# Performance work log

Hardware: AMD Instinct MI355X
Metric: run time of the kernel (lower is better)

## Reference

```python
import jax, jax.numpy as jnp
import numpy as np

N_NODES = 50000
N_EDGES = 1600000
NFEAT = 512
NHID = 64
H1 = 8      # nheads[0]
H2 = 1      # nheads[1]
NCLASS = 16
ALPHA = 0.2  # leaky_relu negative slope


def setup_inputs() -> dict:
    key = jax.random.key(0)
    ks = jax.random.split(key, 6)
    x = jax.random.normal(ks[0], (N_NODES, NFEAT), jnp.float32)
    edge_index = jax.random.randint(ks[1], (2, N_EDGES), 0, N_NODES, jnp.int32)

    def glorot(k, shape):
        fan_in, fan_out = shape[-2], shape[-1]
        std = (2.0 / (fan_in + fan_out)) ** 0.5
        return jax.random.normal(k, shape, jnp.float32) * std

    W1 = glorot(ks[2], (H1, NFEAT, NHID))
    a1 = jax.random.normal(ks[3], (H1, 2 * NHID), jnp.float32) * 0.1
    W2 = glorot(ks[4], (H2, NHID * H1, NCLASS))
    a2 = jax.random.normal(ks[5], (H2, 2 * NCLASS), jnp.float32) * 0.1
    return {"x": x, "edge_index": edge_index, "W1": W1, "a1": a1, "W2": W2, "a2": a2}


def _spgat_head(x, W, a, src, dst, n_nodes, apply_elu):
    # Sparse GAT head (pyGAT SpGraphAttentionLayer, eval mode / no dropout).
    h = x @ W                              # [N, F']
    f = W.shape[1]
    # a . [h_src || h_dst] decomposed into per-node scores (same math, no [E,2F'] concat)
    s_src = h @ a[:f]                      # [N]
    s_dst = h @ a[f:]                      # [N]
    logits = s_src[src] + s_dst[dst]       # [E]
    e = jnp.exp(-jax.nn.leaky_relu(logits, ALPHA))  # edge_e = exp(-leakyrelu(...)) > 0
    rowsum = jax.ops.segment_sum(e, src, num_segments=n_nodes)            # [N]
    agg = jax.ops.segment_sum(e[:, None] * h[dst], src, num_segments=n_nodes)  # [N, F']
    h_prime = agg / rowsum[:, None]
    return jax.nn.elu(h_prime) if apply_elu else h_prime


def reference(x, edge_index, W1, a1, W2, a2):
    src, dst = edge_index[0], edge_index[1]
    n = x.shape[0]
    # Layer 1: H1 heads, concat=True (elu inside each head), concatenated on features
    h = jnp.concatenate(
        [_spgat_head(x, W1[i], a1[i], src, dst, n, True) for i in range(W1.shape[0])],
        axis=1,
    )  # [N, H1*NHID]
    # Layer 2: H2 heads, concat=False, stacked then averaged
    outs = jnp.stack(
        [_spgat_head(h, W2[i], a2[i], src, dst, n, False) for i in range(W2.shape[0])],
        axis=2,
    )  # [N, NCLASS, H2]
    out = jnp.mean(outs, axis=2)
    return jax.nn.log_softmax(jax.nn.elu(out), axis=1)
```

## Files before the change

### kernel.cpp

```cpp
#include <hip/hip_runtime.h>

#define NN 50000
#define NE 1600000
#define NFEAT 512
#define NHID 64
#define H1 8
#define NCLASS 16
#define ALPHA 0.2f

#define BUCKETS 391
#define CAP 6144
#define EPB 4096
#define PASSA_BLKS 391
#define PASSB_BLKS 391
#define PACK_BLKS 1024
#define PACK2_BLKS 32
#define X8_BLKS 6250
#define GEMMB 391
#define NROW_PAD 50048

typedef __attribute__((ext_vector_type(8))) short short8;
typedef __attribute__((ext_vector_type(4))) float floatx4;
typedef __attribute__((ext_vector_type(2))) float floatx2;
typedef __attribute__((ext_vector_type(2))) long longx2;

__device__ __forceinline__ float elu_f(float x) { return x > 0.0f ? x : __expf(x) - 1.0f; }
__device__ __forceinline__ float edge_w(float logit) {
    return __expf(-fmaxf(logit, ALPHA * logit));
}
__device__ __forceinline__ ushort f2bf(float f) {
    uint u = __float_as_uint(f);
    return (ushort)((u + 0x7FFFu + ((u >> 16) & 1)) >> 16);
}
__device__ __forceinline__ uint packbf2(float lo, float hi) {
    return (uint)f2bf(lo) | ((uint)f2bf(hi) << 16);
}
__device__ __forceinline__ float bf2f(ushort v) { return __uint_as_float((uint)v << 16); }
__device__ __forceinline__ unsigned char f2fp8(float v) {
    return (unsigned char)(__builtin_amdgcn_cvt_pk_fp8_f32(v, v, 0, false) & 0xFF);
}
__device__ __forceinline__ uint pack4fp8(float a, float b, float c, float d) {
    uint u = __builtin_amdgcn_cvt_pk_fp8_f32(a, b, 0, false);
    return __builtin_amdgcn_cvt_pk_fp8_f32(c, d, u, true);
}

#define GLD16(g, l)                                                              \
    __builtin_amdgcn_global_load_lds(                                            \
        (const __attribute__((address_space(1))) unsigned int*)(g),              \
        (__attribute__((address_space(3))) unsigned int*)(l), 16, 0, 0)

__device__ __forceinline__ int scan256x(int v, int tid, int* wsum, int* tot) {
    int s = v;
#pragma unroll
    for (int o = 1; o < 64; o <<= 1) {
        int u = __shfl_up(s, o);
        if ((tid & 63) >= o) s += u;
    }
    __syncthreads();
    if ((tid & 63) == 63) wsum[tid >> 6] = s;
    __syncthreads();
    int off = 0, t = 0;
#pragma unroll
    for (int i = 0; i < 4; i++) {
        int x = wsum[i];
        if (i < (tid >> 6)) off += x;
        t += x;
    }
    *tot = t;
    return s - v + off;
}

__device__ __forceinline__ int scan512x(int v, int tid, int* wsum, int* tot) {
    int s = v;
#pragma unroll
    for (int o = 1; o < 64; o <<= 1) {
        int u = __shfl_up(s, o);
        if ((tid & 63) >= o) s += u;
    }
    __syncthreads();
    if ((tid & 63) == 63) wsum[tid >> 6] = s;
    __syncthreads();
    int off = 0, t = 0;
#pragma unroll
    for (int i = 0; i < 8; i++) {
        int x = wsum[i];
        if (i < (tid >> 6)) off += x;
        t += x;
    }
    *tot = t;
    return s - v + off;
}

__global__ __launch_bounds__(256) void prep_k(const float* __restrict__ W1,
                                              unsigned char* __restrict__ Wt8,
                                              const float* __restrict__ W2,
                                              ushort* __restrict__ W2tb,
                                              const float* __restrict__ x,
                                              unsigned char* x8,
                                              const int* __restrict__ ei,
                                              int* __restrict__ bucket_cnt,
                                              uint* __restrict__ staging) {
    int b = blockIdx.x;
    if (b < PACK_BLKS) {
        int i = b * 256 + threadIdx.x;
        int c = i >> 9, o = i & 511;
        int c6 = o >> 6, qhi = (o >> 4) & 3, kb = (o >> 3) & 1, bb = o & 7;
        int quad = qhi ^ ((c >> 1) & 3);
        int k = c6 * 64 + kb * 32 + quad * 8 + bb;
        Wt8[i] = f2fp8(W1[((c >> 6) * 512 + k) * 64 + (c & 63)]);
        return;
    }
    if (b < PACK_BLKS + PACK2_BLKS) {
        int i = (b - PACK_BLKS) * 256 + threadIdx.x;
        int c = i >> 9, f = i & 511;
        W2tb[i] = f2bf(W2[f * 16 + c]);
        return;
    }
    if (b < PACK_BLKS + PACK2_BLKS + X8_BLKS) {
        int i = (b - PACK_BLKS - PACK2_BLKS) * 256 + threadIdx.x;
        int row = i >> 5;
        int o0 = (i & 31) * 16;
        int c6 = o0 >> 6;
        int qhi = (o0 >> 4) & 3;
        int quad = qhi ^ ((row >> 1) & 3);
        const float* xp = x + (size_t)row * 512 + c6 * 64 + quad * 8;
        float4 v0 = *(const float4*)xp;
        float4 v1 = *(const float4*)(xp + 4);
        float4 v2 = *(const float4*)(xp + 32);
        float4 v3 = *(const float4*)(xp + 36);
        uint4 ov;
        ov.x = pack4fp8(v0.x, v0.y, v0.z, v0.w);
        ov.y = pack4fp8(v1.x, v1.y, v1.z, v1.w);
        ov.z = pack4fp8(v2.x, v2.y, v2.z, v2.w);
        ov.w = pack4fp8(v3.x, v3.y, v3.z, v3.w);
        *(uint4*)(x8 + (size_t)row * 512 + o0) = ov;
        return;
    }
    __shared__ int histA[BUCKETS];
    __shared__ int exclA[BUCKETS];
    __shared__ int baseA[BUCKETS];
    __shared__ int wsumA[4];
    __shared__ uint ebuf[EPB];
    const int blk = b - PACK_BLKS - PACK2_BLKS - X8_BLKS;
    const int t = threadIdx.x;
    const int e0 = blk * EPB;
    const int cntb = min(EPB, NE - e0);
    for (int i = t; i < BUCKETS; i += 256) histA[i] = 0;
    __syncthreads();
    int br[16]; uint pay[16];
#pragma unroll
    for (int i = 0; i < 16; i++) {
        int e = e0 + i * 256 + t;
        br[i] = -1;
        if (e < NE) {
            int s = ei[e], d = ei[NE + e];
            int bu = s >> 7;
            pay[i] = ((uint)bu << 23) | ((uint)(s & 127) << 16) | (uint)d;
            br[i] = (bu << 12) | atomicAdd(&histA[bu], 1);
        }
    }
    __syncthreads();
    int tot0, tot1;
    int v0 = histA[t];
    int v1 = (t + 256 < BUCKETS) ? histA[t + 256] : 0;
    int p0 = scan256x(v0, t, wsumA, &tot0);
    int p1 = scan256x(v1, t, wsumA, &tot1);
    exclA[t] = p0;
    if (t + 256 < BUCKETS) exclA[t + 256] = p1 + tot0;
    __syncthreads();
    for (int i = t; i < BUCKETS; i += 256) {
        int c = histA[i];
        if (c > 0) baseA[i] = atomicAdd(&bucket_cnt[i], c);
    }
#pragma unroll
    for (int i = 0; i < 16; i++)
        if (br[i] >= 0) ebuf[exclA[br[i] >> 12] + (br[i] & 4095)] = pay[i];
    __syncthreads();
    for (int j = t; j < cntb; j += 256) {
        uint v = ebuf[j];
        int bu = v >> 23;
        int pos = baseA[bu] + (j - exclA[bu]);
        staging[(size_t)bu * CAP + pos] = v;
    }
}

__global__ __launch_bounds__(512) void passb_gemm1_k(const int* __restrict__ bucket_cnt,
                                                     const uint* __restrict__ staging,
                                                     ushort* __restrict__ csru,
                                                     int* __restrict__ rowptr,
                                                     const unsigned char* __restrict__ Wt8,
                                                     const float* __restrict__ a1,
                                                     unsigned char* h8x8,
                                                     float* __restrict__ s1s,
                                                     float* __restrict__ s1d) {
    __shared__ unsigned char shmem[40960];
    const int tid = threadIdx.x;

    if (blockIdx.x < PASSB_BLKS) {
        int* hist2 = (int*)shmem;
        int* excl2 = hist2 + 128;
        int* cur2 = excl2 + 128;
        int* wsum2 = cur2 + 128;
        __shared__ int sbs;
        const int b = blockIdx.x;
        const int cnt = bucket_cnt[b];
        const uint* sg = staging + (size_t)b * CAP;
        if (tid < 128) { hist2[tid] = 0; cur2[tid] = 0; }
        if (tid < 64) {
            int c[7]; int s0 = 0;
#pragma unroll
            for (int i = 0; i < 7; i++) {
                int bi = tid * 7 + i;
                c[i] = (bi < BUCKETS) ? bucket_cnt[bi] : 0;
                s0 += c[i];
            }
            int sc = s0;
#pragma unroll
            for (int o = 1; o < 64; o <<= 1) {
                int u = __shfl_up(sc, o);
                if (tid >= o) sc += u;
            }
            int run = sc - s0;
            if (tid == b / 7) {
                int part = run;
                for (int i = 0; i < b % 7; i++) part += c[i];
                sbs = part;
            }
        }
        if (b == 0 && tid == 0) rowptr[NN] = NE;
        __syncthreads();
        const int sbase = sbs;
        for (int e = tid; e < cnt; e += 512) atomicAdd(&hist2[(sg[e] >> 16) & 127], 1);
        __syncthreads();
        int v = (tid < 128) ? hist2[tid] : 0;
        int tot;
        int ex = scan512x(v, tid, wsum2, &tot);
        if (tid < 128) {
            excl2[tid] = ex;
            int n = b * 128 + tid;
            if (n < NN) rowptr[n] = sbase + ex;
        }
        __syncthreads();
        for (int e = tid; e < cnt; e += 512) {
            uint u = sg[e];
            int sl = (u >> 16) & 127;
            int pos = excl2[sl] + atomicAdd(&cur2[sl], 1);
            csru[sbase + pos] = (ushort)(u & 0xFFFF);
        }
        return;
    }

    unsigned char* As = shmem;
    unsigned char* Bs = shmem + 8192;
    const int gb = blockIdx.x - PASSB_BLKS;
    const int row0 = gb * 128;
    const int wv = tid >> 6, lane = tid & 63;
    const int l16 = lane & 15, quad = lane >> 4;
    const int qoff = ((quad ^ ((l16 >> 1) & 3)) << 4);
    const int mA = wv * 16 + (lane >> 2);
    const int offA = (lane & 3) * 16;
    const unsigned char* gA = h8x8 + (size_t)(row0 + mA) * 512 + offA;
    const unsigned char* gB0 = Wt8 + (size_t)(0 * 128 + mA) * 512 + offA;
    const unsigned char* gB1 = Wt8 + (size_t)(1 * 128 + mA) * 512 + offA;
    const unsigned char* gB2 = Wt8 + (size_t)(2 * 128 + mA) * 512 + offA;
    const unsigned char* gB3 = Wt8 + (size_t)(3 * 128 + mA) * 512 + offA;

    floatx4 acc[32];
#pragma unroll
    for (int ct = 0; ct < 32; ct++) acc[ct] = (floatx4){0.f, 0.f, 0.f, 0.f};

    for (int k0 = 0; k0 < 512; k0 += 64) {
        GLD16(gA + k0, As + wv * 1024);
        GLD16(gB0 + k0, Bs + wv * 1024);
        GLD16(gB1 + k0, Bs + 8192 + wv * 1024);
        GLD16(gB2 + k0, Bs + 16384 + wv * 1024);
        GLD16(gB3 + k0, Bs + 24576 + wv * 1024);
        __syncthreads();
        longx2 av = *(const longx2*)(As + (wv * 16 + l16) * 64 + qoff);
        const unsigned char* bp = Bs + l16 * 64 + qoff;
#pragma unroll
        for (int ct = 0; ct < 32; ct++) {
            longx2 bv = *(const longx2*)(bp + ct * 1024);
            acc[ct] = __builtin_amdgcn_mfma_f32_16x16x32_fp8_fp8(av.x, bv.x, acc[ct], 0, 0, 0);
            acc[ct] = __builtin_amdgcn_mfma_f32_16x16x32_fp8_fp8(av.y, bv.y, acc[ct], 0, 0, 0);
        }
        __syncthreads();
    }

    const int rbase = row0 + wv * 16 + quad * 4;
#pragma unroll
    for (int hh = 0; hh < 8; hh++) {
        float ss[4] = {0.f, 0.f, 0.f, 0.f}, sd[4] = {0.f, 0.f, 0.f, 0.f};
#pragma unroll
        for (int c4 = 0; c4 < 4; c4++) {
            int ct = hh * 4 + c4;
            int colg = ct * 16 + l16;
            float avs = a1[hh * 128 + c4 * 16 + l16];
            float avd = a1[hh * 128 + 64 + c4 * 16 + l16];
#pragma unroll
            for (int r = 0; r < 4; r++) {
                float v = acc[ct][r];
                ss[r] += v * avs;
                sd[r] += v * avd;
                int row = rbase + r;
                if (row < NN) h8x8[(size_t)row * 512 + colg] = f2fp8(v);
            }
        }
#pragma unroll
        for (int r = 0; r < 4; r++) {
            float a_ = ss[r], b_ = sd[r];
#pragma unroll
            for (int o = 1; o < 16; o <<= 1) {
                a_ += __shfl_xor(a_, o);
                b_ += __shfl_xor(b_, o);
            }
            int row = rbase + r;
            if (l16 == 0 && row < NN) {
                s1s[row * 8 + hh] = a_;
                s1d[row * 8 + hh] = b_;
            }
        }
    }
}

__global__ __launch_bounds__(256) void agg1f_k(const int* __restrict__ rowptr,
                                               const ushort* __restrict__ csru,
                                               const float* __restrict__ s1s,
                                               const float* __restrict__ s1d,
                                               const uint2* __restrict__ hb8,
                                               const ushort* __restrict__ W2tb,
                                               const float* __restrict__ a2,
                                               ushort* __restrict__ h2b,
                                               float* __restrict__ s2s,
                                               float* __restrict__ s2d) {
    __shared__ ushort Ash[16 * 512];
    unsigned char* ashb = (unsigned char*)Ash;
    const int tid = threadIdx.x;
    const int wv = tid >> 6, lane = tid & 63;
    const int n0 = blockIdx.x * 4;
    const int n = n0 + wv;
    const int head8 = lane >> 3;
    const int hb = head8 << 3;
    const int esub = lane & 7;
    const int beg = rowptr[n];
    const int deg = rowptr[n + 1] - beg;
    const float ssrc = s1s[n * 8 + head8];
    floatx2 acc[4] = {};
    float rsum = 0.f;

    const int G = (deg + 7) >> 3;
    const int dm1 = deg - 1;
    if (G > 0) {
        int dA = csru[beg + min(esub, dm1)];
        float tw = s1d[dA * 8 + head8];
        for (int g = 0; g < G; g++) {
            uint2 v[8];
#pragma unroll
            for (int j = 0; j < 8; j++) {
                int dj = __shfl(dA, j);
                v[j] = hb8[(uint)dj * 64 + lane];
            }
            int dAn = csru[beg + min(g * 8 + 8 + esub, dm1)];
            float twn = s1d[dAn * 8 + head8];
            float w = (g * 8 + esub <= dm1) ? edge_w(ssrc + tw) : 0.f;
            rsum += w;
#pragma unroll
            for (int j = 0; j < 8; j++) {
                float wj = __shfl(w, hb + j);
                floatx2 w2 = (floatx2){wj, wj};
                acc[0] += w2 * __builtin_amdgcn_cvt_pk_f32_fp8(v[j].x, false);
                acc[1] += w2 * __builtin_amdgcn_cvt_pk_f32_fp8(v[j].x, true);
                acc[2] += w2 * __builtin_amdgcn_cvt_pk_f32_fp8(v[j].y, false);
                acc[3] += w2 * __builtin_amdgcn_cvt_pk_f32_fp8(v[j].y, true);
            }
            dA = dAn;
            tw = twn;
        }
    }

    rsum += __shfl_xor(rsum, 1);
    rsum += __shfl_xor(rsum, 2);
    rsum += __shfl_xor(rsum, 4);
    float inv = 1.0f / rsum;
    uint4 o;
    o.x = packbf2(elu_f(acc[0][0] * inv), elu_f(acc[0][1] * inv));
    o.y = packbf2(elu_f(acc[1][0] * inv), elu_f(acc[1][1] * inv));
    o.z = packbf2(elu_f(acc[2][0] * inv), elu_f(acc[2][1] * inv));
    o.w = packbf2(elu_f(acc[3][0] * inv), elu_f(acc[3][1] * inv));
    *(uint4*)(ashb + wv * 1024 + ((lane * 16) ^ (wv << 4))) = o;
    __syncthreads();

    if (wv == 0) {
        const int l16 = lane & 15, q = lane >> 4;
        floatx4 c2 = (floatx4){0.f, 0.f, 0.f, 0.f};
#pragma unroll
        for (int s = 0; s < 16; s++) {
            short8 af = *(const short8*)(ashb + l16 * 1024 +
                                         ((s * 64 + q * 16) ^ ((l16 & 7) << 4)));
            short8 bf = *(const short8*)(W2tb + l16 * 512 + s * 32 + q * 8);
            c2 = __builtin_amdgcn_mfma_f32_16x16x32_bf16(af, bf, c2, 0, 0, 0);
        }
        if (q == 0) {
#pragma unroll
            for (int r = 0; r < 4; r++) h2b[(size_t)(n0 + r) * 16 + l16] = f2bf(c2[r]);
        }
#pragma unroll
        for (int r = 0; r < 4; r++) {
            float ssv = c2[r] * a2[l16];
            float sdv = c2[r] * a2[16 + l16];
#pragma unroll
            for (int oo = 1; oo < 16; oo <<= 1) {
                ssv += __shfl_xor(ssv, oo);
                sdv += __shfl_xor(sdv, oo);
            }
            if (lane == 0) { s2s[n0 + r] = ssv; s2d[n0 + r] = sdv; }
        }
    }
}

__global__ __launch_bounds__(256) void agg2_k(const int* __restrict__ rowptr,
                                              const ushort* __restrict__ csru,
                                              const float* __restrict__ s2s,
                                              const float* __restrict__ s2d,
                                              const ushort* __restrict__ h2b,
                                              float* __restrict__ out) {
    const int n = (blockIdx.x * 256 + threadIdx.x) >> 6;
    const int lane = threadIdx.x & 63;
    if (n >= NN) return;
    const int beg = rowptr[n], end = rowptr[n + 1];
    const float sn = s2s[n];
    const int sub = lane >> 4, f = lane & 15;
    float acc = 0.f, rsum = 0.f;
    int e = beg + sub;
    for (; e + 12 < end; e += 16) {
        int d0 = csru[e], d1 = csru[e + 4], d2 = csru[e + 8], d3 = csru[e + 12];
        float t0 = s2d[d0], t1 = s2d[d1], t2 = s2d[d2], t3 = s2d[d3];
        float g0 = bf2f(h2b[(uint)d0 * 16 + f]), g1 = bf2f(h2b[(uint)d1 * 16 + f]);
        float g2 = bf2f(h2b[(uint)d2 * 16 + f]), g3 = bf2f(h2b[(uint)d3 * 16 + f]);
        float w0 = edge_w(sn + t0), w1 = edge_w(sn + t1);
        float w2 = edge_w(sn + t2), w3 = edge_w(sn + t3);
        acc += w0 * g0 + w1 * g1 + w2 * g2 + w3 * g3;
        rsum += w0 + w1 + w2 + w3;
    }
    for (; e < end; e += 4) {
        int d0 = csru[e];
        float w0 = edge_w(sn + s2d[d0]);
        acc += w0 * bf2f(h2b[(uint)d0 * 16 + f]);
        rsum += w0;
    }
    acc += __shfl_down(acc, 32);
    acc += __shfl_down(acc, 16);
    rsum += __shfl_down(rsum, 32);
    rsum += __shfl_down(rsum, 16);
    if (lane < 16) {
        float v = elu_f(acc / rsum);
        float m = v;
#pragma unroll
        for (int o = 8; o > 0; o >>= 1) m = fmaxf(m, __shfl_xor(m, o));
        float ex = __expf(v - m), s = ex;
#pragma unroll
        for (int o = 8; o > 0; o >>= 1) s += __shfl_xor(s, o);
        out[(size_t)n * 16 + f] = v - (__logf(s) + m);
    }
}

extern "C" void kernel_launch(void* const* d_in, const int* in_sizes, int n_in,
                              void* d_out, int out_size, void* d_ws, size_t ws_size,
                              hipStream_t stream) {
    const float* x  = (const float*)d_in[0];
    const int*   ei = (const int*)d_in[1];
    const float* W1 = (const float*)d_in[2];
    const float* a1 = (const float*)d_in[3];
    const float* W2 = (const float*)d_in[4];
    const float* a2 = (const float*)d_in[5];
    float* out = (float*)d_out;

    unsigned char* h8  = (unsigned char*)d_ws;
    unsigned char* Wt8 = h8 + (size_t)NROW_PAD * 512;
    ushort* W2tb  = (ushort*)(Wt8 + 512 * 512);
    float* s1s    = (float*)(W2tb + 8192);
    float* s1d    = s1s + (size_t)NN * H1;
    int* rowptr   = (int*)(s1d + (size_t)NN * H1);
    int* bucket_cnt   = rowptr + 50056;
    int* bucket_start = bucket_cnt + 512;
    ushort* csru  = (ushort*)(bucket_start + 512);
    ushort* h2b   = csru + NE;
    float* s2s    = (float*)(h2b + (size_t)NN * 16);
    float* s2d    = s2s + NN;
    uint* staging = (uint*)(s2d + NN);

    hipMemsetAsync(bucket_cnt, 0, 512 * sizeof(int), stream);

    prep_k<<<PACK_BLKS + PACK2_BLKS + X8_BLKS + PASSA_BLKS, 256, 0, stream>>>(
        W1, Wt8, W2, W2tb, x, h8, ei, bucket_cnt, staging);
    passb_gemm1_k<<<PASSB_BLKS + GEMMB, 512, 0, stream>>>(bucket_cnt, staging, csru, rowptr,
                                                          Wt8, a1, h8, s1s, s1d);
    agg1f_k<<<NN / 4, 256, 0, stream>>>(rowptr, csru, s1s, s1d,
                                        (const uint2*)h8, W2tb, a2, h2b, s2s, s2d);
    agg2_k<<<(NN + 3) / 4, 256, 0, stream>>>(rowptr, csru, s2s, s2d, h2b, out);
}
```

Baseline: 396.7 us.

## Pad per-node CSR segments to multiples of eight with per-bucket bases and vector index loads

```diff
diff --git a/kernel.cpp b/kernel.cpp
--- a/kernel.cpp
+++ b/kernel.cpp
@@ -9,7 +9,8 @@
 #define ALPHA 0.2f
 
 #define BUCKETS 391
-#define CAP 6144
+#define CAPS 5120
+#define CAP2 5632
 #define EPB 4096
 #define PASSA_BLKS 391
 #define PASSB_BLKS 391
@@ -180,7 +181,7 @@
         uint v = ebuf[j];
         int bu = v >> 23;
         int pos = baseA[bu] + (j - exclA[bu]);
-        staging[(size_t)bu * CAP + pos] = v;
+        staging[(size_t)bu * CAPS + pos] = v;
     }
 }
 
@@ -188,6 +189,7 @@
                                                      const uint* __restrict__ staging,
                                                      ushort* __restrict__ csru,
                                                      int* __restrict__ rowptr,
+                                                     int* __restrict__ degarr,
                                                      const unsigned char* __restrict__ Wt8,
                                                      const float* __restrict__ a1,
                                                      unsigned char* h8x8,
@@ -201,51 +203,29 @@
         int* excl2 = hist2 + 128;
         int* cur2 = excl2 + 128;
         int* wsum2 = cur2 + 128;
-        __shared__ int sbs;
         const int b = blockIdx.x;
         const int cnt = bucket_cnt[b];
-        const uint* sg = staging + (size_t)b * CAP;
+        const uint* sg = staging + (size_t)b * CAPS;
+        const int bbase = b * CAP2;
         if (tid < 128) { hist2[tid] = 0; cur2[tid] = 0; }
-        if (tid < 64) {
-            int c[7]; int s0 = 0;
-#pragma unroll
-            for (int i = 0; i < 7; i++) {
-                int bi = tid * 7 + i;
-                c[i] = (bi < BUCKETS) ? bucket_cnt[bi] : 0;
-                s0 += c[i];
-            }
-            int sc = s0;
-#pragma unroll
-            for (int o = 1; o < 64; o <<= 1) {
-                int u = __shfl_up(sc, o);
-                if (tid >= o) sc += u;
-            }
-            int run = sc - s0;
-            if (tid == b / 7) {
-                int part = run;
-                for (int i = 0; i < b % 7; i++) part += c[i];
-                sbs = part;
-            }
-        }
-        if (b == 0 && tid == 0) rowptr[NN] = NE;
         __syncthreads();
-        const int sbase = sbs;
         for (int e = tid; e < cnt; e += 512) atomicAdd(&hist2[(sg[e] >> 16) & 127], 1);
         __syncthreads();
-        int v = (tid < 128) ? hist2[tid] : 0;
+        int dn = (tid < 128) ? hist2[tid] : 0;
+        int v = (dn + 7) & ~7;
         int tot;
         int ex = scan512x(v, tid, wsum2, &tot);
         if (tid < 128) {
             excl2[tid] = ex;
-            int n = b * 128 + tid;
-            if (n < NN) rowptr[n] = sbase + ex;
+            int nn_ = b * 128 + tid;
+            if (nn_ < NN) { rowptr[nn_] = bbase + ex; degarr[nn_] = dn; }
         }
         __syncthreads();
         for (int e = tid; e < cnt; e += 512) {
             uint u = sg[e];
             int sl = (u >> 16) & 127;
             int pos = excl2[sl] + atomicAdd(&cur2[sl], 1);
-            csru[sbase + pos] = (ushort)(u & 0xFFFF);
+            csru[bbase + pos] = (ushort)(u & 0xFFFF);
         }
         return;
     }
@@ -324,6 +304,7 @@
 }
 
 __global__ __launch_bounds__(256) void agg1f_k(const int* __restrict__ rowptr,
+                                               const int* __restrict__ degarr,
                                                const ushort* __restrict__ csru,
                                                const float* __restrict__ s1s,
                                                const float* __restrict__ s1d,
@@ -342,39 +323,37 @@
     const int head8 = lane >> 3;
     const int hb = head8 << 3;
     const int esub = lane & 7;
-    const int beg = rowptr[n];
-    const int deg = rowptr[n + 1] - beg;
+    const int beg = __builtin_amdgcn_readfirstlane(rowptr[n]);
+    const int degu = __builtin_amdgcn_readfirstlane(degarr[n]);
     const float ssrc = s1s[n * 8 + head8];
     floatx2 acc[4] = {};
     float rsum = 0.f;
 
-    const int G = (deg + 7) >> 3;
-    const int dm1 = deg - 1;
+    const int G = (degu + 7) >> 3;
+    const uint4* cq = (const uint4*)(csru + beg);
     if (G > 0) {
-        int dA = csru[beg + min(esub, dm1)];
-        float tw = s1d[dA * 8 + head8];
+        uint4 dp = cq[0];
         for (int g = 0; g < G; g++) {
-            uint2 v[8];
+            uint4 dpn = (g + 1 < G) ? cq[g + 1] : dp;
+            uint wpair = (esub & 4) ? ((esub & 2) ? dp.w : dp.z)
+                                    : ((esub & 2) ? dp.y : dp.x);
+            uint dme = (wpair >> ((esub & 1) << 4)) & 0xFFFFu;
+            float w = (g * 8 + esub < degu) ? edge_w(ssrc + s1d[dme * 8 + head8]) : 0.f;
+            rsum += w;
+            uint dw0 = dp.x, dw1 = dp.y, dw2 = dp.z, dw3 = dp.w;
 #pragma unroll
             for (int j = 0; j < 8; j++) {
-                int dj = __shfl(dA, j);
-                v[j] = hb8[(uint)dj * 64 + lane];
-            }
-            int dAn = csru[beg + min(g * 8 + 8 + esub, dm1)];
-            float twn = s1d[dAn * 8 + head8];
-            float w = (g * 8 + esub <= dm1) ? edge_w(ssrc + tw) : 0.f;
-            rsum += w;
-#pragma unroll
-            for (int j = 0; j < 8; j++) {
+                uint dword = (j < 2) ? dw0 : (j < 4) ? dw1 : (j < 6) ? dw2 : dw3;
+                uint dj = (dword >> ((j & 1) << 4)) & 0xFFFFu;
+                uint2 vj = hb8[(size_t)dj * 64 + lane];
                 float wj = __shfl(w, hb + j);
                 floatx2 w2 = (floatx2){wj, wj};
-                acc[0] += w2 * __builtin_amdgcn_cvt_pk_f32_fp8(v[j].x, false);
-                acc[1] += w2 * __builtin_amdgcn_cvt_pk_f32_fp8(v[j].x, true);
-                acc[2] += w2 * __builtin_amdgcn_cvt_pk_f32_fp8(v[j].y, false);
-                acc[3] += w2 * __builtin_amdgcn_cvt_pk_f32_fp8(v[j].y, true);
+                acc[0] += w2 * __builtin_amdgcn_cvt_pk_f32_fp8(vj.x, false);
+                acc[1] += w2 * __builtin_amdgcn_cvt_pk_f32_fp8(vj.x, true);
+                acc[2] += w2 * __builtin_amdgcn_cvt_pk_f32_fp8(vj.y, false);
+                acc[3] += w2 * __builtin_amdgcn_cvt_pk_f32_fp8(vj.y, true);
             }
-            dA = dAn;
-            tw = twn;
+            dp = dpn;
         }
     }
 
@@ -419,6 +398,7 @@
 }
 
 __global__ __launch_bounds__(256) void agg2_k(const int* __restrict__ rowptr,
+                                              const int* __restrict__ degarr,
                                               const ushort* __restrict__ csru,
                                               const float* __restrict__ s2s,
                                               const float* __restrict__ s2d,
@@ -427,7 +407,7 @@
     const int n = (blockIdx.x * 256 + threadIdx.x) >> 6;
     const int lane = threadIdx.x & 63;
     if (n >= NN) return;
-    const int beg = rowptr[n], end = rowptr[n + 1];
+    const int beg = rowptr[n], end = beg + degarr[n];
     const float sn = s2s[n];
     const int sub = lane >> 4, f = lane & 15;
     float acc = 0.f, rsum = 0.f;
@@ -481,10 +461,10 @@
     float* s1s    = (float*)(W2tb + 8192);
     float* s1d    = s1s + (size_t)NN * H1;
     int* rowptr   = (int*)(s1d + (size_t)NN * H1);
-    int* bucket_cnt   = rowptr + 50056;
-    int* bucket_start = bucket_cnt + 512;
-    ushort* csru  = (ushort*)(bucket_start + 512);
-    ushort* h2b   = csru + NE;
+    int* degarr   = rowptr + NROW_PAD;
+    int* bucket_cnt = degarr + NROW_PAD;
+    ushort* csru  = (ushort*)(bucket_cnt + 512);
+    ushort* h2b   = csru + (size_t)BUCKETS * CAP2;
     float* s2s    = (float*)(h2b + (size_t)NN * 16);
     float* s2d    = s2s + NN;
     uint* staging = (uint*)(s2d + NN);
@@ -493,9 +473,10 @@
 
     prep_k<<<PACK_BLKS + PACK2_BLKS + X8_BLKS + PASSA_BLKS, 256, 0, stream>>>(
         W1, Wt8, W2, W2tb, x, h8, ei, bucket_cnt, staging);
-    passb_gemm1_k<<<PASSB_BLKS + GEMMB, 512, 0, stream>>>(bucket_cnt, staging, csru, rowptr,
+    passb_gemm1_k<<<PASSB_BLKS + GEMMB, 512, 0, stream>>>(bucket_cnt, staging, csru,
+                                                          rowptr, degarr,
                                                           Wt8, a1, h8, s1s, s1d);
-    agg1f_k<<<NN / 4, 256, 0, stream>>>(rowptr, csru, s1s, s1d,
+    agg1f_k<<<NN / 4, 256, 0, stream>>>(rowptr, degarr, csru, s1s, s1d,
                                         (const uint2*)h8, W2tb, a2, h2b, s2s, s2d);
-    agg2_k<<<(NN + 3) / 4, 256, 0, stream>>>(rowptr, csru, s2s, s2d, h2b, out);
-}
+    agg2_k<<<(NN + 3) / 4, 256, 0, stream>>>(rowptr, degarr, csru, s2s, s2d, h2b, out);
+}
```

Result: slower. 444.2 us (+12.0%).

## Double-buffer LDS tiles in fused FP8 GEMM1 to overlap loads with MFMA

Applied to the files above, without the earlier changes.

```diff
diff --git a/kernel.cpp b/kernel.cpp
--- a/kernel.cpp
+++ b/kernel.cpp
@@ -193,7 +193,7 @@
                                                      unsigned char* h8x8,
                                                      float* __restrict__ s1s,
                                                      float* __restrict__ s1d) {
-    __shared__ unsigned char shmem[40960];
+    __shared__ unsigned char shmem[81920];
     const int tid = threadIdx.x;
 
     if (blockIdx.x < PASSB_BLKS) {
@@ -251,7 +251,7 @@
     }
 
     unsigned char* As = shmem;
-    unsigned char* Bs = shmem + 8192;
+    unsigned char* Bs = shmem + 16384;
     const int gb = blockIdx.x - PASSB_BLKS;
     const int row0 = gb * 128;
     const int wv = tid >> 6, lane = tid & 63;
@@ -265,26 +265,40 @@
     const unsigned char* gB2 = Wt8 + (size_t)(2 * 128 + mA) * 512 + offA;
     const unsigned char* gB3 = Wt8 + (size_t)(3 * 128 + mA) * 512 + offA;
 
+#define STAGE_T(k0, p)                                           \
+    {                                                            \
+        GLD16(gA + (k0), As + (p)*8192 + wv * 1024);             \
+        GLD16(gB0 + (k0), Bs + (p)*32768 + wv * 1024);           \
+        GLD16(gB1 + (k0), Bs + (p)*32768 + 8192 + wv * 1024);    \
+        GLD16(gB2 + (k0), Bs + (p)*32768 + 16384 + wv * 1024);   \
+        GLD16(gB3 + (k0), Bs + (p)*32768 + 24576 + wv * 1024);   \
+    }
+
     floatx4 acc[32];
 #pragma unroll
     for (int ct = 0; ct < 32; ct++) acc[ct] = (floatx4){0.f, 0.f, 0.f, 0.f};
 
-    for (int k0 = 0; k0 < 512; k0 += 64) {
-        GLD16(gA + k0, As + wv * 1024);
-        GLD16(gB0 + k0, Bs + wv * 1024);
-        GLD16(gB1 + k0, Bs + 8192 + wv * 1024);
-        GLD16(gB2 + k0, Bs + 16384 + wv * 1024);
-        GLD16(gB3 + k0, Bs + 24576 + wv * 1024);
-        __syncthreads();
-        longx2 av = *(const longx2*)(As + (wv * 16 + l16) * 64 + qoff);
-        const unsigned char* bp = Bs + l16 * 64 + qoff;
+    STAGE_T(0, 0);
+    for (int t = 0; t < 8; t++) {
+        if (t < 7) STAGE_T((t + 1) * 64, (t + 1) & 1);
+        if (t < 7) asm volatile("s_waitcnt vmcnt(5)" ::: "memory");
+        else       asm volatile("s_waitcnt vmcnt(0)" ::: "memory");
+        __builtin_amdgcn_sched_barrier(0);
+        __builtin_amdgcn_s_barrier();
+        __builtin_amdgcn_sched_barrier(0);
+        const unsigned char* Ap = As + (t & 1) * 8192;
+        const unsigned char* Bp = Bs + (t & 1) * 32768;
+        longx2 av = *(const longx2*)(Ap + (wv * 16 + l16) * 64 + qoff);
+        const unsigned char* bp = Bp + l16 * 64 + qoff;
 #pragma unroll
         for (int ct = 0; ct < 32; ct++) {
             longx2 bv = *(const longx2*)(bp + ct * 1024);
             acc[ct] = __builtin_amdgcn_mfma_f32_16x16x32_fp8_fp8(av.x, bv.x, acc[ct], 0, 0, 0);
             acc[ct] = __builtin_amdgcn_mfma_f32_16x16x32_fp8_fp8(av.y, bv.y, acc[ct], 0, 0, 0);
         }
-        __syncthreads();
+        __builtin_amdgcn_sched_barrier(0);
+        __builtin_amdgcn_s_barrier();
+        __builtin_amdgcn_sched_barrier(0);
     }
 
     const int rbase = row0 + wv * 16 + quad * 4;
```

Result: no change. 395.9 us (-0.2%).
